# Performance work log

Hardware: AMD Instinct MI355X
Metric: run time of the kernel (lower is better)

The kernel has to match this reference:

```python
import jax, jax.numpy as jnp
import numpy as np

EMBED = 1024
HEAD = 64

def setup_inputs() -> dict:
    key = jax.random.key(0)
    k1, k2, k3, k4 = jax.random.split(key, 4)
    embeddings = jax.random.normal(k1, (8, 2048, EMBED), dtype=jnp.float32)
    # nn.Linear weight is [out, in]; we store transposed [in, out] for x @ W
    scale = 1.0 / np.sqrt(EMBED)
    Wk = jax.random.uniform(k2, (EMBED, HEAD), dtype=jnp.float32, minval=-scale, maxval=scale)
    Wq = jax.random.uniform(k3, (EMBED, HEAD), dtype=jnp.float32, minval=-scale, maxval=scale)
    Wv = jax.random.uniform(k4, (EMBED, HEAD), dtype=jnp.float32, minval=-scale, maxval=scale)
    return {"embeddings": embeddings, "Wq": Wq, "Wk": Wk, "Wv": Wv}

def reference(embeddings, Wq, Wk, Wv):
    B, S, D = embeddings.shape
    q = embeddings @ Wq  # [B,S,H]
    k = embeddings @ Wk
    v = embeddings @ Wv
    norm = k.shape[-1] ** (-0.5)
    scores = jnp.einsum('bqh,bkh->bqk', q, k) * norm  # [B,S,S]
    causal = jnp.tril(jnp.ones((S, S), dtype=bool))
    scores = jnp.where(causal, scores, -jnp.inf)
    weights = jax.nn.softmax(scores, axis=-1)
    # dropout p=0.0 (eval-equivalent): identity
    return jnp.einsum('bqk,bkh->bqh', weights, v)
```

## Files before the change

kernel.cpp:

```cpp
#include <hip/hip_runtime.h>

#define SEQ   2048
#define NBATCH 8
#define EMB   1024
#define HD    64
#define QKVSZ (NBATCH * SEQ * HD)
#define WTSZ  (3 * HD * EMB)
#define KSTR  72
#define VSTR  72
#define PSTR  72
#define PSLOT 1088

typedef __attribute__((ext_vector_type(8))) short bf16x8;
typedef __attribute__((ext_vector_type(4))) float f32x4;

__device__ inline unsigned short f2b(float f) {
  union { float f; unsigned int i; } u; u.f = f;
  unsigned int r = (u.i + 0x7FFFu + ((u.i >> 16) & 1u)) >> 16;
  return (unsigned short)r;
}

__global__ __launch_bounds__(256) void wtrans_kernel(const float* __restrict__ wq,
                                                     const float* __restrict__ wk,
                                                     const float* __restrict__ wv,
                                                     unsigned short* __restrict__ wt) {
  int i = blockIdx.x * 256 + threadIdx.x;
  int kb  = i / 12288;
  int rem = i - kb * 12288;
  int m   = rem >> 12;
  int c   = (rem >> 6) & 63;
  int kd  = rem & 63;
  const float* src = (m == 0) ? wq : ((m == 1) ? wk : wv);
  int d = kb * 64 + kd;
  wt[i] = f2b(src[d * 64 + c]);
}

__global__ __launch_bounds__(256, 4) void qkv_proj_kernel(const float* __restrict__ emb,
                                                          const unsigned short* __restrict__ wt,
                                                          unsigned short* __restrict__ qkv) {
  __shared__ __align__(16) unsigned short Ab[2][32 * 64];
  __shared__ __align__(16) unsigned short Wb[2][96 * 64];

  const int t    = threadIdx.x;
  const int wave = t >> 6;
  const int lane = t & 63;
  const int quad = lane >> 4;
  const int l16  = lane & 15;
  const int bx = blockIdx.x;
  const int rt = bx >> 1;
  const int ch = bx & 1;
  const int wr = wave >> 1;
  const int wc = wave & 1;

  const float* aBase = emb + (size_t)rt * 32 * EMB;
  const unsigned short* wBase = wt + ch * 6144;

  f32x4 acc[3];
#pragma unroll
  for (int j = 0; j < 3; j++) acc[j] = (f32x4){0.f, 0.f, 0.f, 0.f};

  f32x4 pa[2];
  bf16x8 pw[3];

#pragma unroll
  for (int j = 0; j < 2; j++) {
    int u = t + j * 256;
    pa[j] = *(const f32x4*)(aBase + (size_t)(u >> 4) * EMB + (u & 15) * 4);
  }
#pragma unroll
  for (int j = 0; j < 3; j++) {
    int u = t + j * 256;
    pw[j] = *(const bf16x8*)(wBase + u * 8);
  }
#pragma unroll
  for (int j = 0; j < 2; j++) {
    int u = t + j * 256;
    int row = u >> 4, kq = u & 15;
    unsigned int lo = (unsigned int)f2b(pa[j][0]) | ((unsigned int)f2b(pa[j][1]) << 16);
    unsigned int hi = (unsigned int)f2b(pa[j][2]) | ((unsigned int)f2b(pa[j][3]) << 16);
    uint2 pk; pk.x = lo; pk.y = hi;
    *(uint2*)((char*)&Ab[0][0] + row * 128 + ((kq * 8) ^ ((row & 7) << 4))) = pk;
  }
#pragma unroll
  for (int j = 0; j < 3; j++) {
    int u = t + j * 256;
    int coll = u >> 3, kd8 = u & 7;
    *(bf16x8*)((char*)&Wb[0][0] + coll * 128 + ((kd8 ^ (coll & 7)) << 4)) = pw[j];
  }
  __syncthreads();

#pragma unroll 2
  for (int kb = 0; kb < 16; kb++) {
    const int cur = kb & 1;

    if (kb < 15) {
#pragma unroll
      for (int j = 0; j < 2; j++) {
        int u = t + j * 256;
        pa[j] = *(const f32x4*)(aBase + (size_t)(u >> 4) * EMB + (kb + 1) * 64 + (u & 15) * 4);
      }
#pragma unroll
      for (int j = 0; j < 3; j++) {
        int u = t + j * 256;
        pw[j] = *(const bf16x8*)(wBase + (kb + 1) * 12288 + u * 8);
      }
    }

    const int arow = wr * 16 + l16;
#pragma unroll
    for (int kh = 0; kh < 2; kh++) {
      bf16x8 af = *(const bf16x8*)((const char*)&Ab[cur][0] + arow * 128 +
                                   ((kh * 64 + quad * 16) ^ ((arow & 7) << 4)));
#pragma unroll
      for (int j = 0; j < 3; j++) {
        const int coll = (wc * 3 + j) * 16 + l16;
        bf16x8 wf = *(const bf16x8*)((const char*)&Wb[cur][0] + coll * 128 +
                                     ((kh * 64 + quad * 16) ^ ((coll & 7) << 4)));
        acc[j] = __builtin_amdgcn_mfma_f32_16x16x32_bf16(af, wf, acc[j], 0, 0, 0);
      }
    }

    if (kb < 15) {
      const int nb = cur ^ 1;
#pragma unroll
      for (int j = 0; j < 2; j++) {
        int u = t + j * 256;
        int row = u >> 4, kq = u & 15;
        unsigned int lo = (unsigned int)f2b(pa[j][0]) | ((unsigned int)f2b(pa[j][1]) << 16);
        unsigned int hi = (unsigned int)f2b(pa[j][2]) | ((unsigned int)f2b(pa[j][3]) << 16);
        uint2 pk; pk.x = lo; pk.y = hi;
        *(uint2*)((char*)&Ab[nb][0] + row * 128 + ((kq * 8) ^ ((row & 7) << 4))) = pk;
      }
#pragma unroll
      for (int j = 0; j < 3; j++) {
        int u = t + j * 256;
        int coll = u >> 3, kd8 = u & 7;
        *(bf16x8*)((char*)&Wb[nb][0] + coll * 128 + ((kd8 ^ (coll & 7)) << 4)) = pw[j];
      }
      __syncthreads();
    }
  }

#pragma unroll
  for (int j = 0; j < 3; j++) {
    int gc = ch * 96 + (wc * 3 + j) * 16 + l16;
    int m  = gc >> 6, cm = gc & 63;
#pragma unroll
    for (int r = 0; r < 4; r++) {
      int row = rt * 32 + wr * 16 + quad * 4 + r;
      qkv[(size_t)m * QKVSZ + (size_t)row * HD + cm] = f2b(acc[j][r]);
    }
  }
}

__global__ __launch_bounds__(64, 2) void attn_split(const unsigned short* __restrict__ qkv,
                                                    float* __restrict__ part,
                                                    float* __restrict__ out) {
  __shared__ __align__(16) unsigned short Ksh[64 * KSTR];
  __shared__ __align__(16) unsigned short Vt[64 * VSTR];
  __shared__ __align__(16) unsigned short Psh[16 * PSTR];

  const int t = threadIdx.x;
  const int quad = t >> 4;
  const int l16  = t & 15;
  const int idx = blockIdx.x;
  const int b   = blockIdx.y;
  const int qt  = (idx < 128) ? idx : (64 + (idx - 128));
  const int c   = (idx < 128) ? 0 : 1;
  const int q0  = qt * 16;
  const int kdiag = qt >> 2;
  const int t0 = c * 16;
  const int t1 = (c == 0) ? min(15, kdiag) : kdiag;

  const unsigned short* qg = qkv;
  const unsigned short* kg = qkv + QKVSZ;
  const unsigned short* vg = qkv + 2 * QKVSZ;

  const unsigned short* qptr = qg + ((size_t)(b * SEQ + q0 + l16)) * HD + quad * 8;
  const bf16x8 qf0 = *(const bf16x8*)qptr;
  const bf16x8 qf1 = *(const bf16x8*)(qptr + 32);

  f32x4 o0 = {0,0,0,0}, o1 = {0,0,0,0}, o2 = {0,0,0,0}, o3 = {0,0,0,0};
  float mst[4] = {-INFINITY, -INFINITY, -INFINITY, -INFINITY};
  float lst[4] = {0.f, 0.f, 0.f, 0.f};
  const float sc = 0.125f * 1.44269504088896f;

  bf16x8 kpre[8], vpre[8];
  {
    const bf16x8* ks = (const bf16x8*)(kg + ((size_t)(b * SEQ + t0 * 64)) * HD);
#pragma unroll
    for (int i = 0; i < 8; i++) kpre[i] = ks[t + i * 64];
    const bf16x8* vs = (const bf16x8*)(vg + ((size_t)(b * SEQ + t0 * 64 + t)) * HD);
#pragma unroll
    for (int i = 0; i < 8; i++) vpre[i] = vs[i];
  }

  for (int kb = t0; kb <= t1; kb++) {
#pragma unroll
    for (int i = 0; i < 8; i++) {
      int u = t + i * 64;
      *(bf16x8*)(Ksh + (u >> 3) * KSTR + (u & 7) * 8) = kpre[i];
    }
#pragma unroll
    for (int i = 0; i < 8; i++)
#pragma unroll
      for (int j = 0; j < 8; j++)
        Vt[(i * 8 + j) * VSTR + t] = (unsigned short)vpre[i][j];
    __syncthreads();

    if (kb < t1) {
      const bf16x8* ks = (const bf16x8*)(kg + ((size_t)(b * SEQ + (kb + 1) * 64)) * HD);
#pragma unroll
      for (int i = 0; i < 8; i++) kpre[i] = ks[t + i * 64];
      const bf16x8* vs = (const bf16x8*)(vg + ((size_t)(b * SEQ + (kb + 1) * 64 + t)) * HD);
#pragma unroll
      for (int i = 0; i < 8; i++) vpre[i] = vs[i];
    }

    f32x4 s[4];
#pragma unroll
    for (int kt = 0; kt < 4; kt++) {
      bf16x8 kf0 = *(const bf16x8*)(Ksh + (kt * 16 + l16) * KSTR + quad * 8);
      bf16x8 kf1 = *(const bf16x8*)(Ksh + (kt * 16 + l16) * KSTR + 32 + quad * 8);
      f32x4 z = {0.f, 0.f, 0.f, 0.f};
      z = __builtin_amdgcn_mfma_f32_16x16x32_bf16(qf0, kf0, z, 0, 0, 0);
      z = __builtin_amdgcn_mfma_f32_16x16x32_bf16(qf1, kf1, z, 0, 0, 0);
      s[kt] = z;
    }

    if (kb == kdiag) {
#pragma unroll
      for (int r = 0; r < 4; r++) {
        int rowg = q0 + quad * 4 + r;
#pragma unroll
        for (int kt = 0; kt < 4; kt++) {
          int col = kb * 64 + kt * 16 + l16;
          float v = s[kt][r] * sc;
          s[kt][r] = (col > rowg) ? -INFINITY : v;
        }
      }
    } else {
#pragma unroll
      for (int r = 0; r < 4; r++)
#pragma unroll
        for (int kt = 0; kt < 4; kt++) s[kt][r] *= sc;
    }

    float alpha[4];
#pragma unroll
    for (int r = 0; r < 4; r++) {
      float mx = fmaxf(fmaxf(s[0][r], s[1][r]), fmaxf(s[2][r], s[3][r]));
#pragma unroll
      for (int off = 1; off < 16; off <<= 1) mx = fmaxf(mx, __shfl_xor(mx, off, 64));
      float mnew = fmaxf(mst[r], mx);
      alpha[r] = exp2f(mst[r] - mnew);
      mst[r] = mnew;
    }
#pragma unroll
    for (int r = 0; r < 4; r++) {
      float sm = 0.f;
#pragma unroll
      for (int kt = 0; kt < 4; kt++) {
        float p = exp2f(s[kt][r] - mst[r]);
        s[kt][r] = p;
        sm += p;
      }
#pragma unroll
      for (int off = 1; off < 16; off <<= 1) sm += __shfl_xor(sm, off, 64);
      lst[r] = lst[r] * alpha[r] + sm;
    }
#pragma unroll
    for (int r = 0; r < 4; r++) { o0[r] *= alpha[r]; o1[r] *= alpha[r]; o2[r] *= alpha[r]; o3[r] *= alpha[r]; }

#pragma unroll
    for (int kt = 0; kt < 4; kt++)
#pragma unroll
      for (int r = 0; r < 4; r++)
        Psh[(quad * 4 + r) * PSTR + kt * 16 + l16] = f2b(s[kt][r]);
    __syncthreads();

#pragma unroll
    for (int kc = 0; kc < 2; kc++) {
      bf16x8 pf = *(const bf16x8*)(Psh + l16 * PSTR + kc * 32 + quad * 8);
      bf16x8 vf0 = *(const bf16x8*)(Vt + (0 + l16) * VSTR + kc * 32 + quad * 8);
      bf16x8 vf1 = *(const bf16x8*)(Vt + (16 + l16) * VSTR + kc * 32 + quad * 8);
      bf16x8 vf2 = *(const bf16x8*)(Vt + (32 + l16) * VSTR + kc * 32 + quad * 8);
      bf16x8 vf3 = *(const bf16x8*)(Vt + (48 + l16) * VSTR + kc * 32 + quad * 8);
      o0 = __builtin_amdgcn_mfma_f32_16x16x32_bf16(pf, vf0, o0, 0, 0, 0);
      o1 = __builtin_amdgcn_mfma_f32_16x16x32_bf16(pf, vf1, o1, 0, 0, 0);
      o2 = __builtin_amdgcn_mfma_f32_16x16x32_bf16(pf, vf2, o2, 0, 0, 0);
      o3 = __builtin_amdgcn_mfma_f32_16x16x32_bf16(pf, vf3, o3, 0, 0, 0);
    }
    __syncthreads();
  }

  if (qt < 64) {
#pragma unroll
    for (int r = 0; r < 4; r++) {
      float inv = 1.f / lst[r];
      int rowg = q0 + quad * 4 + r;
      size_t ob = ((size_t)(b * SEQ + rowg)) * HD + l16;
      out[ob + 0]  = o0[r] * inv;
      out[ob + 16] = o1[r] * inv;
      out[ob + 32] = o2[r] * inv;
      out[ob + 48] = o3[r] * inv;
    }
  } else {
    float* ps = part + ((size_t)((b * 64 + (qt - 64)) * 2 + c)) * PSLOT;
#pragma unroll
    for (int r = 0; r < 4; r++) {
      int row = quad * 4 + r;
      ps[row * 64 + 0  + l16] = o0[r];
      ps[row * 64 + 16 + l16] = o1[r];
      ps[row * 64 + 32 + l16] = o2[r];
      ps[row * 64 + 48 + l16] = o3[r];
      if (l16 == 0) {
        ps[1024 + row] = mst[r];
        ps[1040 + row] = lst[r];
      }
    }
  }
}

__global__ __launch_bounds__(64) void attn_merge(const float* __restrict__ part,
                                                 float* __restrict__ out) {
  const int h  = threadIdx.x;
  const int qx = blockIdx.x;
  const int b  = blockIdx.y;
  const float* p0 = part + ((size_t)((b * 64 + qx) * 2 + 0)) * PSLOT;
  const float* p1 = p0 + PSLOT;
#pragma unroll 4
  for (int r = 0; r < 16; r++) {
    float m0 = p0[1024 + r], l0 = p0[1040 + r];
    float m1 = p1[1024 + r], l1 = p1[1040 + r];
    float M  = fmaxf(m0, m1);
    float e0 = exp2f(m0 - M), e1 = exp2f(m1 - M);
    float L  = l0 * e0 + l1 * e1;
    float o  = (p0[r * 64 + h] * e0 + p1[r * 64 + h] * e1) / L;
    out[((size_t)(b * SEQ + (64 + qx) * 16 + r)) * HD + h] = o;
  }
}

extern "C" void kernel_launch(void* const* d_in, const int* in_sizes, int n_in,
                              void* d_out, int out_size, void* d_ws, size_t ws_size,
                              hipStream_t stream) {
  const float* emb = (const float*)d_in[0];
  const float* wq  = (const float*)d_in[1];
  const float* wk  = (const float*)d_in[2];
  const float* wv  = (const float*)d_in[3];
  unsigned short* ws  = (unsigned short*)d_ws;
  unsigned short* wt  = ws;
  unsigned short* qkv = ws + WTSZ;
  float* part = (float*)(ws + WTSZ + 3 * QKVSZ);

  hipLaunchKernelGGL(wtrans_kernel,   dim3(WTSZ / 256), dim3(256), 0, stream, wq, wk, wv, wt);
  hipLaunchKernelGGL(qkv_proj_kernel, dim3(1024),       dim3(256), 0, stream, emb, wt, qkv);
  hipLaunchKernelGGL(attn_split,      dim3(192, 8),     dim3(64),  0, stream, qkv, part, (float*)d_out);
  hipLaunchKernelGGL(attn_merge,      dim3(64, 8),      dim3(64),  0, stream, part, (float*)d_out);
}
```

Before: 170.6 us.

## Store V transposed from projection kernel, swizzle LDS tiles, rebalance split

The projection kernel now writes V in a head-major transposed layout by staging it through shared memory, so the attention kernel can load V^T with vector loads. This removes the per-element scalar transpose into LDS inside the attention loop. Padded LDS strides are replaced with XOR-swizzled 128-byte rows for K, V^T and P to avoid bank conflicts without padding. The two-way split of long query tiles now divides key blocks in half rather than at a fixed boundary, for better load balance. The cost is an extra LDS staging step and two syncthreads in the projection epilogue.

New measurement: 161.5 us. -5.3%, faster.

```diff
diff --git a/kernel.cpp b/kernel.cpp
--- a/kernel.cpp
+++ b/kernel.cpp
@@ -6,9 +6,6 @@
 #define HD    64
 #define QKVSZ (NBATCH * SEQ * HD)
 #define WTSZ  (3 * HD * EMB)
-#define KSTR  72
-#define VSTR  72
-#define PSTR  72
 #define PSLOT 1088
 
 typedef __attribute__((ext_vector_type(8))) short bf16x8;
@@ -144,33 +141,63 @@
 #pragma unroll
   for (int j = 0; j < 3; j++) {
     int gc = ch * 96 + (wc * 3 + j) * 16 + l16;
-    int m  = gc >> 6, cm = gc & 63;
-#pragma unroll
-    for (int r = 0; r < 4; r++) {
-      int row = rt * 32 + wr * 16 + quad * 4 + r;
-      qkv[(size_t)m * QKVSZ + (size_t)row * HD + cm] = f2b(acc[j][r]);
-    }
+    if (gc < 128) {
+      int m  = gc >> 6, cm = gc & 63;
+#pragma unroll
+      for (int r = 0; r < 4; r++) {
+        int row = rt * 32 + wr * 16 + quad * 4 + r;
+        qkv[(size_t)m * QKVSZ + (size_t)row * HD + cm] = f2b(acc[j][r]);
+      }
+    }
+  }
+
+  if (ch == 1) {
+    __syncthreads();
+    unsigned short* Vsh = (unsigned short*)&Ab[0][0];
+#pragma unroll
+    for (int j = 0; j < 3; j++) {
+      int gc = 96 + (wc * 3 + j) * 16 + l16;
+      if (gc >= 128) {
+        int h = gc - 128;
+#pragma unroll
+        for (int r = 0; r < 4; r++)
+          Vsh[h * 40 + wr * 16 + quad * 4 + r] = f2b(acc[j][r]);
+      }
+    }
+    __syncthreads();
+    int h  = t >> 2;
+    int sq = (t & 3) * 8;
+    int row0 = rt * 32;
+    int b    = row0 >> 11;
+    int seq0 = row0 & 2047;
+    bf16x8 vv = *(const bf16x8*)(Vsh + h * 40 + sq);
+    *(bf16x8*)(qkv + 2 * (size_t)QKVSZ + ((size_t)(b * 64 + h)) * SEQ + seq0 + sq) = vv;
   }
 }
 
 __global__ __launch_bounds__(64, 2) void attn_split(const unsigned short* __restrict__ qkv,
                                                     float* __restrict__ part,
                                                     float* __restrict__ out) {
-  __shared__ __align__(16) unsigned short Ksh[64 * KSTR];
-  __shared__ __align__(16) unsigned short Vt[64 * VSTR];
-  __shared__ __align__(16) unsigned short Psh[16 * PSTR];
+  __shared__ __align__(16) unsigned short Ksh[64 * 64];
+  __shared__ __align__(16) unsigned short Vt[64 * 64];
+  __shared__ __align__(16) unsigned short Psh[16 * 64];
 
   const int t = threadIdx.x;
   const int quad = t >> 4;
   const int l16  = t & 15;
   const int idx = blockIdx.x;
   const int b   = blockIdx.y;
-  const int qt  = (idx < 128) ? idx : (64 + (idx - 128));
+  const int qt  = (idx < 128) ? idx : (idx - 64);
   const int c   = (idx < 128) ? 0 : 1;
   const int q0  = qt * 16;
   const int kdiag = qt >> 2;
-  const int t0 = c * 16;
-  const int t1 = (c == 0) ? min(15, kdiag) : kdiag;
+  int t0, t1;
+  if (qt < 64) { t0 = 0; t1 = kdiag; }
+  else {
+    int n0 = (kdiag + 2) >> 1;
+    t0 = c ? n0 : 0;
+    t1 = c ? kdiag : (n0 - 1);
+  }
 
   const unsigned short* qg = qkv;
   const unsigned short* kg = qkv + QKVSZ;
@@ -187,41 +214,41 @@
 
   bf16x8 kpre[8], vpre[8];
   {
-    const bf16x8* ks = (const bf16x8*)(kg + ((size_t)(b * SEQ + t0 * 64)) * HD);
-#pragma unroll
-    for (int i = 0; i < 8; i++) kpre[i] = ks[t + i * 64];
-    const bf16x8* vs = (const bf16x8*)(vg + ((size_t)(b * SEQ + t0 * 64 + t)) * HD);
-#pragma unroll
-    for (int i = 0; i < 8; i++) vpre[i] = vs[i];
-  }
-
-  for (int kb = t0; kb <= t1; kb++) {
+    const unsigned short* kgb = kg + ((size_t)(b * SEQ + t0 * 64)) * HD;
 #pragma unroll
     for (int i = 0; i < 8; i++) {
       int u = t + i * 64;
-      *(bf16x8*)(Ksh + (u >> 3) * KSTR + (u & 7) * 8) = kpre[i];
-    }
-#pragma unroll
-    for (int i = 0; i < 8; i++)
-#pragma unroll
-      for (int j = 0; j < 8; j++)
-        Vt[(i * 8 + j) * VSTR + t] = (unsigned short)vpre[i][j];
+      kpre[i] = *(const bf16x8*)(kgb + (size_t)(u >> 3) * HD + (u & 7) * 8);
+      vpre[i] = *(const bf16x8*)(vg + ((size_t)(b * 64 + (u >> 3))) * SEQ + t0 * 64 + (u & 7) * 8);
+    }
+  }
+
+  for (int kb = t0; kb <= t1; kb++) {
+#pragma unroll
+    for (int i = 0; i < 8; i++) {
+      int u = t + i * 64;
+      int row = u >> 3, sb = (u & 7) * 16;
+      *(bf16x8*)((char*)Ksh + row * 128 + (sb ^ ((row & 7) << 4))) = kpre[i];
+      *(bf16x8*)((char*)Vt  + row * 128 + (sb ^ ((row & 7) << 4))) = vpre[i];
+    }
     __syncthreads();
 
     if (kb < t1) {
-      const bf16x8* ks = (const bf16x8*)(kg + ((size_t)(b * SEQ + (kb + 1) * 64)) * HD);
-#pragma unroll
-      for (int i = 0; i < 8; i++) kpre[i] = ks[t + i * 64];
-      const bf16x8* vs = (const bf16x8*)(vg + ((size_t)(b * SEQ + (kb + 1) * 64 + t)) * HD);
-#pragma unroll
-      for (int i = 0; i < 8; i++) vpre[i] = vs[i];
+      const unsigned short* kgb = kg + ((size_t)(b * SEQ + (kb + 1) * 64)) * HD;
+#pragma unroll
+      for (int i = 0; i < 8; i++) {
+        int u = t + i * 64;
+        kpre[i] = *(const bf16x8*)(kgb + (size_t)(u >> 3) * HD + (u & 7) * 8);
+        vpre[i] = *(const bf16x8*)(vg + ((size_t)(b * 64 + (u >> 3))) * SEQ + (kb + 1) * 64 + (u & 7) * 8);
+      }
     }
 
     f32x4 s[4];
 #pragma unroll
     for (int kt = 0; kt < 4; kt++) {
-      bf16x8 kf0 = *(const bf16x8*)(Ksh + (kt * 16 + l16) * KSTR + quad * 8);
-      bf16x8 kf1 = *(const bf16x8*)(Ksh + (kt * 16 + l16) * KSTR + 32 + quad * 8);
+      int row = kt * 16 + l16;
+      bf16x8 kf0 = *(const bf16x8*)((char*)Ksh + row * 128 + ((quad * 16) ^ ((row & 7) << 4)));
+      bf16x8 kf1 = *(const bf16x8*)((char*)Ksh + row * 128 + ((64 + quad * 16) ^ ((row & 7) << 4)));
       f32x4 z = {0.f, 0.f, 0.f, 0.f};
       z = __builtin_amdgcn_mfma_f32_16x16x32_bf16(qf0, kf0, z, 0, 0, 0);
       z = __builtin_amdgcn_mfma_f32_16x16x32_bf16(qf1, kf1, z, 0, 0, 0);
@@ -275,21 +302,28 @@
 #pragma unroll
     for (int kt = 0; kt < 4; kt++)
 #pragma unroll
-      for (int r = 0; r < 4; r++)
-        Psh[(quad * 4 + r) * PSTR + kt * 16 + l16] = f2b(s[kt][r]);
+      for (int r = 0; r < 4; r++) {
+        int row = quad * 4 + r;
+        *(unsigned short*)((char*)Psh + row * 128 + ((kt * 32 + l16 * 2) ^ ((row & 7) << 4))) = f2b(s[kt][r]);
+      }
     __syncthreads();
 
 #pragma unroll
     for (int kc = 0; kc < 2; kc++) {
-      bf16x8 pf = *(const bf16x8*)(Psh + l16 * PSTR + kc * 32 + quad * 8);
-      bf16x8 vf0 = *(const bf16x8*)(Vt + (0 + l16) * VSTR + kc * 32 + quad * 8);
-      bf16x8 vf1 = *(const bf16x8*)(Vt + (16 + l16) * VSTR + kc * 32 + quad * 8);
-      bf16x8 vf2 = *(const bf16x8*)(Vt + (32 + l16) * VSTR + kc * 32 + quad * 8);
-      bf16x8 vf3 = *(const bf16x8*)(Vt + (48 + l16) * VSTR + kc * 32 + quad * 8);
-      o0 = __builtin_amdgcn_mfma_f32_16x16x32_bf16(pf, vf0, o0, 0, 0, 0);
-      o1 = __builtin_amdgcn_mfma_f32_16x16x32_bf16(pf, vf1, o1, 0, 0, 0);
-      o2 = __builtin_amdgcn_mfma_f32_16x16x32_bf16(pf, vf2, o2, 0, 0, 0);
-      o3 = __builtin_amdgcn_mfma_f32_16x16x32_bf16(pf, vf3, o3, 0, 0, 0);
+      bf16x8 pf = *(const bf16x8*)((char*)Psh + l16 * 128 + ((kc * 64 + quad * 16) ^ ((l16 & 7) << 4)));
+#pragma unroll
+      for (int ht = 0; ht < 1; ht++) {}
+      {
+        int r0 = 0 * 16 + l16, r1 = 1 * 16 + l16, r2 = 2 * 16 + l16, r3 = 3 * 16 + l16;
+        bf16x8 vf0 = *(const bf16x8*)((char*)Vt + r0 * 128 + ((kc * 64 + quad * 16) ^ ((r0 & 7) << 4)));
+        bf16x8 vf1 = *(const bf16x8*)((char*)Vt + r1 * 128 + ((kc * 64 + quad * 16) ^ ((r1 & 7) << 4)));
+        bf16x8 vf2 = *(const bf16x8*)((char*)Vt + r2 * 128 + ((kc * 64 + quad * 16) ^ ((r2 & 7) << 4)));
+        bf16x8 vf3 = *(const bf16x8*)((char*)Vt + r3 * 128 + ((kc * 64 + quad * 16) ^ ((r3 & 7) << 4)));
+        o0 = __builtin_amdgcn_mfma_f32_16x16x32_bf16(pf, vf0, o0, 0, 0, 0);
+        o1 = __builtin_amdgcn_mfma_f32_16x16x32_bf16(pf, vf1, o1, 0, 0, 0);
+        o2 = __builtin_amdgcn_mfma_f32_16x16x32_bf16(pf, vf2, o2, 0, 0, 0);
+        o3 = __builtin_amdgcn_mfma_f32_16x16x32_bf16(pf, vf3, o3, 0, 0, 0);
+      }
     }
     __syncthreads();
   }
```
